# Optimization experiments

Measured on AMD Instinct MI355X. Metric: run time of the kernel, lower is better.

The kernel has to match this reference:

```python
import jax
import jax.numpy as jnp
from jax import lax
import numpy as np

DIM = 64
EPS = 1e-5
DN = ('NCDHW', 'OIDHW', 'NCDHW')


def setup_inputs() -> dict:
    key = jax.random.key(0)
    ks = jax.random.split(key, 4)
    x = jax.random.normal(ks[0], (2, DIM, 64, 64, 64), dtype=jnp.float32)
    gamma = jnp.ones((DIM,), jnp.float32)
    beta = jnp.zeros((DIM,), jnp.float32)
    w0 = jax.random.normal(ks[1], (DIM, 1, 5, 5, 5), jnp.float32) * 0.1
    b0 = jnp.zeros((DIM,), jnp.float32)
    ws = jax.random.normal(ks[2], (DIM, 1, 7, 7, 7), jnp.float32) * 0.05
    bs = jnp.zeros((DIM,), jnp.float32)
    w1 = jax.random.normal(ks[3], (DIM, DIM, 1, 1, 1), jnp.float32) * 0.1
    b1 = jnp.zeros((DIM,), jnp.float32)
    return {"x": x, "gamma": gamma, "beta": beta, "w0": w0, "b0": b0,
            "ws": ws, "bs": bs, "w1": w1, "b1": b1}


def _cb(b):
    # broadcast per-channel vector over NCDHW
    return b.reshape(1, -1, 1, 1, 1)


def reference(x, gamma, beta, w0, b0, ws, bs, w1, b1):
    dim = x.shape[1]
    # BatchNorm (training mode, biased variance) over N, D, H, W per channel
    mean = jnp.mean(x, axis=(0, 2, 3, 4), keepdims=True)
    var = jnp.var(x, axis=(0, 2, 3, 4), keepdims=True)
    xn = (x - mean) * lax.rsqrt(var + EPS) * _cb(gamma) + _cb(beta)
    # depthwise conv3d k=5, pad=2 (same)
    attn = lax.conv_general_dilated(xn, w0, (1, 1, 1), [(2, 2)] * 3,
                                    feature_group_count=dim,
                                    dimension_numbers=DN) + _cb(b0)
    # dilated depthwise conv3d k=7, dilation=3, pad=9 (same)
    attn = lax.conv_general_dilated(attn, ws, (1, 1, 1), [(9, 9)] * 3,
                                    rhs_dilation=(3, 3, 3),
                                    feature_group_count=dim,
                                    dimension_numbers=DN) + _cb(bs)
    # pointwise 1x1x1 conv
    attn = lax.conv_general_dilated(attn, w1, (1, 1, 1), [(0, 0)] * 3,
                                    dimension_numbers=DN) + _cb(b1)
    # gated multiply with residual input (u = x.clone())
    return x * attn
```

## Files before the change

### kernel.cpp

```cpp
#include <hip/hip_runtime.h>
#include <math.h>

#define C_DIM 64
#define N_B 2
#define SPATIAL (64*64*64)
#define PLANE_SZ (64*64)
#define EPSV 1e-5f

__global__ __launch_bounds__(256) void k_stats(const float* __restrict__ x,
                                               float* __restrict__ wsf) {
    int c = blockIdx.x >> 4;
    int part = blockIdx.x & 15;
    int tid = threadIdx.x;
    const int per_part = SPATIAL / 16;
    float s = 0.f, sq = 0.f;
    for (int n = 0; n < N_B; ++n) {
        const float* base = x + ((size_t)(n * C_DIM + c)) * SPATIAL + (size_t)part * per_part;
        const float4* b4 = (const float4*)base;
        #pragma unroll
        for (int it = 0; it < 16; ++it) {
            float4 v = b4[it * 256 + tid];
            s  += v.x + v.y + v.z + v.w;
            sq += v.x*v.x + v.y*v.y + v.z*v.z + v.w*v.w;
        }
    }
    __shared__ float rs[256], rq[256];
    rs[tid] = s; rq[tid] = sq;
    __syncthreads();
    for (int off = 128; off > 0; off >>= 1) {
        if (tid < off) { rs[tid] += rs[tid+off]; rq[tid] += rq[tid+off]; }
        __syncthreads();
    }
    if (tid == 0) {
        atomicAdd(&wsf[c], rs[0]);
        atomicAdd(&wsf[64 + c], rq[0]);
    }
}

__global__ void k_finalize(float* __restrict__ wsf,
                           const float* __restrict__ gamma,
                           const float* __restrict__ beta) {
    int c = threadIdx.x;
    float cnt = (float)(N_B * SPATIAL);
    float mean = wsf[c] / cnt;
    float var = wsf[64 + c] / cnt - mean * mean;
    float sc = gamma[c] * rsqrtf(var + EPSV);
    wsf[128 + c] = sc;
    wsf[192 + c] = beta[c] - mean * sc;
}

#define K2D 12
#define K2H 12
#define K2W 36
__global__ __launch_bounds__(256) void k_conv5(const float* __restrict__ x,
                                               const float* __restrict__ w0,
                                               const float* __restrict__ b0,
                                               const float* __restrict__ wsf,
                                               float* __restrict__ attn0) {
    __shared__ float sh[K2D * K2H * K2W];
    __shared__ float wt[125];
    int tid = threadIdx.x;
    int tx = tid & 31;
    int ty = tid >> 5;
    int wtile = blockIdx.x;
    int dt = blockIdx.y & 7;
    int ht = blockIdx.y >> 3;
    int nc = blockIdx.z;
    int c = nc & 63;
    int w0i = wtile * 32;
    int h0 = ht * 8;
    int d0 = dt * 8;
    const float* xb = x + (size_t)nc * SPATIAL;
    float sc = wsf[128 + c], shv = wsf[192 + c];
    if (tid < 125) wt[tid] = w0[c * 125 + tid];
    for (int idx = tid; idx < K2D * K2H * K2W; idx += 256) {
        int z = idx / (K2H * K2W);
        int rem = idx - z * (K2H * K2W);
        int y = rem / K2W;
        int xw = rem - y * K2W;
        int gd = d0 - 2 + z, gh = h0 - 2 + y, gw = w0i - 2 + xw;
        float v = 0.f;
        if ((unsigned)gd < 64u && (unsigned)gh < 64u && (unsigned)gw < 64u)
            v = xb[(size_t)gd * PLANE_SZ + gh * 64 + gw] * sc + shv;
        sh[idx] = v;
    }
    __syncthreads();
    float acc[8] = {0,0,0,0,0,0,0,0};
    #pragma unroll
    for (int z = 0; z < 12; ++z) {
        #pragma unroll
        for (int j = 0; j < 5; ++j) {
            #pragma unroll
            for (int k = 0; k < 5; ++k) {
                float v = sh[(z * K2H + (ty + j)) * K2W + tx + k];
                #pragma unroll
                for (int i = 0; i < 5; ++i) {
                    int dz = z - i;
                    if (dz >= 0 && dz < 8)
                        acc[dz] += wt[(i * 5 + j) * 5 + k] * v;
                }
            }
        }
    }
    float bias = b0[c];
    float* ob = attn0 + (size_t)nc * SPATIAL + (size_t)(h0 + ty) * 64 + w0i + tx;
    #pragma unroll
    for (int dz = 0; dz < 8; ++dz)
        ob[(size_t)(d0 + dz) * PLANE_SZ] = acc[dz] + bias;
}

#define ROWS7 22
#define COLS7 84

template<int P>
__device__ __forceinline__ void conv7_stage(const float* __restrict__ ab,
                                            const float* __restrict__ wc,
                                            float* __restrict__ sh,
                                            int tid, int hh, int w, int h0,
                                            int j0, int rd, float (&acc)[8]) {
    int m = j0 - 3 + P;
    int z = 3 * m + rd;
    bool zok = (m >= 0) && (z < 64);
    __syncthreads();
    if (zok) {
        const float* pb = ab + (size_t)z * PLANE_SZ;
        #pragma unroll
        for (int k = 0; k < 8; ++k) {
            int idx = k * 256 + tid;
            if (idx < ROWS7 * COLS7) {
                int row = idx / COLS7;
                int col = idx - row * COLS7;
                int gy = h0 - 9 + row;
                int gx = col - 9;
                float v = 0.f;
                if (col < 82 && (unsigned)gy < 64u && (unsigned)gx < 64u)
                    v = pb[gy * 64 + gx];
                sh[idx] = v;
            }
        }
    }
    __syncthreads();
    if (zok) {
        #pragma unroll
        for (int v = 0; v < 7; ++v) {
            float val[7];
            int rb = (hh + 3 * v) * COLS7 + w;
            #pragma unroll
            for (int u = 0; u < 7; ++u) val[u] = sh[rb + 3 * u];
            #pragma unroll
            for (int t = 0; t < 7; ++t) {
                const int q = P - t;
                if (q >= 0 && q < 8) {
                    #pragma unroll
                    for (int u = 0; u < 7; ++u)
                        acc[q] = fmaf(wc[t * 49 + v * 7 + u], val[u], acc[q]);
                }
            }
        }
    }
}

__global__ __launch_bounds__(256) void k_conv7(const float* __restrict__ attn0,
                                               const float* __restrict__ wsv,
                                               const float* __restrict__ bs,
                                               float* __restrict__ attn1) {
    __shared__ float sh[ROWS7 * COLS7];
    int tid = threadIdx.x;
    int w = tid & 63;
    int hh = tid >> 6;
    int ht = blockIdx.x;
    int rd = blockIdx.y % 3;
    int j0 = (blockIdx.y / 3) * 8;
    int nc = blockIdx.z;
    int c = nc & 63;
    int h0 = ht * 4;
    int h = h0 + hh;
    const float* ab = attn0 + (size_t)nc * SPATIAL;
    const float* wc = wsv + c * 343;
    float acc[8] = {0,0,0,0,0,0,0,0};

    conv7_stage< 0>(ab, wc, sh, tid, hh, w, h0, j0, rd, acc);
    conv7_stage< 1>(ab, wc, sh, tid, hh, w, h0, j0, rd, acc);
    conv7_stage< 2>(ab, wc, sh, tid, hh, w, h0, j0, rd, acc);
    conv7_stage< 3>(ab, wc, sh, tid, hh, w, h0, j0, rd, acc);
    conv7_stage< 4>(ab, wc, sh, tid, hh, w, h0, j0, rd, acc);
    conv7_stage< 5>(ab, wc, sh, tid, hh, w, h0, j0, rd, acc);
    conv7_stage< 6>(ab, wc, sh, tid, hh, w, h0, j0, rd, acc);
    conv7_stage< 7>(ab, wc, sh, tid, hh, w, h0, j0, rd, acc);
    conv7_stage< 8>(ab, wc, sh, tid, hh, w, h0, j0, rd, acc);
    conv7_stage< 9>(ab, wc, sh, tid, hh, w, h0, j0, rd, acc);
    conv7_stage<10>(ab, wc, sh, tid, hh, w, h0, j0, rd, acc);
    conv7_stage<11>(ab, wc, sh, tid, hh, w, h0, j0, rd, acc);
    conv7_stage<12>(ab, wc, sh, tid, hh, w, h0, j0, rd, acc);
    conv7_stage<13>(ab, wc, sh, tid, hh, w, h0, j0, rd, acc);

    float bias = bs[c];
    float* ob = attn1 + (size_t)nc * SPATIAL + (size_t)h * 64 + w;
    #pragma unroll
    for (int q = 0; q < 8; ++q) {
        int d = 3 * (j0 + q) + rd;
        if (d < 64)
            ob[(size_t)d * PLANE_SZ] = acc[q] + bias;
    }
}

__global__ __launch_bounds__(256) void k_pointwise(const float* __restrict__ attn1,
                                                   const float* __restrict__ x,
                                                   const float* __restrict__ w1,
                                                   const float* __restrict__ b1,
                                                   float* __restrict__ out) {
    __shared__ float at[64 * 64];
    int tid = threadIdx.x;
    int sl = tid & 63;
    int cg = __builtin_amdgcn_readfirstlane(tid >> 6);
    int s0 = blockIdx.x * 64;
    int n = blockIdx.y;
    const float* a_base = attn1 + (size_t)n * C_DIM * SPATIAL + s0;
    #pragma unroll
    for (int it = 0; it < 16; ++it) {
        int idx = it * 256 + tid;
        int row = idx >> 6;
        at[idx] = a_base[(size_t)row * SPATIAL + sl];
    }
    __syncthreads();
    float acc[16];
    #pragma unroll
    for (int j = 0; j < 16; ++j) acc[j] = 0.f;
    for (int ci = 0; ci < 64; ++ci) {
        float va = at[ci * 64 + sl];
        #pragma unroll
        for (int j = 0; j < 16; ++j) {
            int cc = cg * 16 + j;
            acc[j] += w1[cc * 64 + ci] * va;
        }
    }
    const float* xb = x + (size_t)n * C_DIM * SPATIAL + s0;
    float* ob = out + (size_t)n * C_DIM * SPATIAL + s0;
    #pragma unroll
    for (int j = 0; j < 16; ++j) {
        int cc = cg * 16 + j;
        float attn = acc[j] + b1[cc];
        ob[(size_t)cc * SPATIAL + sl] = xb[(size_t)cc * SPATIAL + sl] * attn;
    }
}

extern "C" void kernel_launch(void* const* d_in, const int* in_sizes, int n_in,
                              void* d_out, int out_size, void* d_ws, size_t ws_size,
                              hipStream_t stream) {
    const float* x     = (const float*)d_in[0];
    const float* gamma = (const float*)d_in[1];
    const float* beta  = (const float*)d_in[2];
    const float* w0    = (const float*)d_in[3];
    const float* b0    = (const float*)d_in[4];
    const float* wsv   = (const float*)d_in[5];
    const float* bs    = (const float*)d_in[6];
    const float* w1    = (const float*)d_in[7];
    const float* b1    = (const float*)d_in[8];
    float* out = (float*)d_out;
    float* wsf = (float*)d_ws;
    float* attn1 = wsf + 256;

    hipMemsetAsync(d_ws, 0, 1024, stream);
    k_stats<<<dim3(1024), dim3(256), 0, stream>>>(x, wsf);
    k_finalize<<<dim3(1), dim3(64), 0, stream>>>(wsf, gamma, beta);
    k_conv5<<<dim3(2, 64, 128), dim3(256), 0, stream>>>(x, w0, b0, wsf, out);
    k_conv7<<<dim3(16, 9, 128), dim3(256), 0, stream>>>(out, wsv, bs, attn1);
    k_pointwise<<<dim3(4096, 2), dim3(256), 0, stream>>>(attn1, x, w1, b1, out);
}
```

Before: 1.316 ms.

## Restructure dilated conv7 as depth-streaming sliding window with double-buffered planes

Rewrites the dilated 7x7x7 depthwise conv so each block owns one (rd, rh) dilation phase of a whole channel. It streams depth planes through double-buffered shared memory and keeps a 7-deep sliding accumulator per output, so every input plane is loaded once instead of once per output tile. Each thread now computes 4 strided rows, which reuses the values it loads across several outputs. The cost is far fewer blocks (9x128) with a large register footprint from 28 accumulators, which may hurt occupancy.

```diff
diff --git a/kernel.cpp b/kernel.cpp
--- a/kernel.cpp
+++ b/kernel.cpp
@@ -109,98 +109,121 @@
         ob[(size_t)(d0 + dz) * PLANE_SZ] = acc[dz] + bias;
 }
 
-#define ROWS7 22
+#define ROWS7 30
 #define COLS7 84
-
-template<int P>
-__device__ __forceinline__ void conv7_stage(const float* __restrict__ ab,
-                                            const float* __restrict__ wc,
-                                            float* __restrict__ sh,
-                                            int tid, int hh, int w, int h0,
-                                            int j0, int rd, float (&acc)[8]) {
-    int m = j0 - 3 + P;
-    int z = 3 * m + rd;
-    bool zok = (m >= 0) && (z < 64);
-    __syncthreads();
-    if (zok) {
-        const float* pb = ab + (size_t)z * PLANE_SZ;
-        #pragma unroll
-        for (int k = 0; k < 8; ++k) {
-            int idx = k * 256 + tid;
-            if (idx < ROWS7 * COLS7) {
-                int row = idx / COLS7;
-                int col = idx - row * COLS7;
-                int gy = h0 - 9 + row;
-                int gx = col - 9;
-                float v = 0.f;
-                if (col < 82 && (unsigned)gy < 64u && (unsigned)gx < 64u)
-                    v = pb[gy * 64 + gx];
-                sh[idx] = v;
-            }
-        }
-    }
-    __syncthreads();
-    if (zok) {
-        #pragma unroll
-        for (int v = 0; v < 7; ++v) {
+#define S7_T 384
+#define S7_ITERS 7
+#define S7_BUF (S7_ITERS * S7_T)
+
+__global__ __launch_bounds__(384, 4) void k_conv7(const float* __restrict__ attn0,
+                                                  const float* __restrict__ wsv,
+                                                  const float* __restrict__ bs,
+                                                  float* __restrict__ attn1) {
+    __shared__ float sh[2 * S7_BUF];
+    int tid = threadIdx.x;
+    int w  = tid & 63;
+    int th = tid >> 6;
+    int rh = blockIdx.x % 3;
+    int rd = blockIdx.x / 3;
+    int nc = blockIdx.y;
+    int c  = nc & 63;
+    const float* ab = attn0 + (size_t)nc * SPATIAL;
+    const float* wc = wsv + c * 343;
+    int M = (66 - rd) / 3;
+    int ah0 = th * 4;
+    int ahmax = (63 - rh) / 3;
+
+    int goff[S7_ITERS];
+    float gmsk[S7_ITERS];
+    #pragma unroll
+    for (int kk = 0; kk < S7_ITERS; ++kk) {
+        int idx = kk * S7_T + tid;
+        int row = idx / COLS7;
+        int e   = idx - row * COLS7;
+        int gy  = 3 * (row - 3) + rh;
+        int gx  = e - 9;
+        bool valid = (row < ROWS7) && ((unsigned)gy < 64u) && ((unsigned)gx < 64u);
+        goff[kk] = valid ? (gy * 64 + gx) : 0;
+        gmsk[kk] = valid ? 1.f : 0.f;
+    }
+
+    float acc[4][7];
+    #pragma unroll
+    for (int k = 0; k < 4; ++k)
+        #pragma unroll
+        for (int s = 0; s < 7; ++s) acc[k][s] = 0.f;
+
+    {
+        const float* pb = ab + (size_t)rd * PLANE_SZ;
+        #pragma unroll
+        for (int kk = 0; kk < S7_ITERS; ++kk)
+            sh[kk * S7_T + tid] = pb[goff[kk]] * gmsk[kk];
+    }
+    __syncthreads();
+
+    float bias = bs[c];
+    float* ob = attn1 + (size_t)nc * SPATIAL + (size_t)rd * PLANE_SZ
+              + (size_t)(3 * ah0 + rh) * 64 + w;
+    int rbase = ah0 * COLS7 + w;
+
+    for (int m = 0; m < M; ++m) {
+        const float* cur = sh + (m & 1) * S7_BUF;
+        float* nxt = sh + ((m + 1) & 1) * S7_BUF;
+        bool more = (m + 1 < M);
+        float r[S7_ITERS];
+        if (more) {
+            const float* pb = ab + (size_t)(3 * (m + 1) + rd) * PLANE_SZ;
+            #pragma unroll
+            for (int kk = 0; kk < S7_ITERS; ++kk)
+                r[kk] = pb[goff[kk]];
+        }
+        #pragma unroll
+        for (int jp = 0; jp < 10; ++jp) {
             float val[7];
-            int rb = (hh + 3 * v) * COLS7 + w;
-            #pragma unroll
-            for (int u = 0; u < 7; ++u) val[u] = sh[rb + 3 * u];
-            #pragma unroll
-            for (int t = 0; t < 7; ++t) {
-                const int q = P - t;
-                if (q >= 0 && q < 8) {
+            #pragma unroll
+            for (int u = 0; u < 7; ++u)
+                val[u] = cur[rbase + jp * COLS7 + 3 * u];
+            #pragma unroll
+            for (int k = 0; k < 4; ++k) {
+                const int v = jp - k;
+                if (v >= 0 && v < 7) {
                     #pragma unroll
-                    for (int u = 0; u < 7; ++u)
-                        acc[q] = fmaf(wc[t * 49 + v * 7 + u], val[u], acc[q]);
+                    for (int s = 0; s < 7; ++s) {
+                        #pragma unroll
+                        for (int u = 0; u < 7; ++u)
+                            acc[k][s] = fmaf(wc[(6 - s) * 49 + v * 7 + u],
+                                             val[u], acc[k][s]);
+                    }
                 }
             }
         }
-    }
-}
-
-__global__ __launch_bounds__(256) void k_conv7(const float* __restrict__ attn0,
-                                               const float* __restrict__ wsv,
-                                               const float* __restrict__ bs,
-                                               float* __restrict__ attn1) {
-    __shared__ float sh[ROWS7 * COLS7];
-    int tid = threadIdx.x;
-    int w = tid & 63;
-    int hh = tid >> 6;
-    int ht = blockIdx.x;
-    int rd = blockIdx.y % 3;
-    int j0 = (blockIdx.y / 3) * 8;
-    int nc = blockIdx.z;
-    int c = nc & 63;
-    int h0 = ht * 4;
-    int h = h0 + hh;
-    const float* ab = attn0 + (size_t)nc * SPATIAL;
-    const float* wc = wsv + c * 343;
-    float acc[8] = {0,0,0,0,0,0,0,0};
-
-    conv7_stage< 0>(ab, wc, sh, tid, hh, w, h0, j0, rd, acc);
-    conv7_stage< 1>(ab, wc, sh, tid, hh, w, h0, j0, rd, acc);
-    conv7_stage< 2>(ab, wc, sh, tid, hh, w, h0, j0, rd, acc);
-    conv7_stage< 3>(ab, wc, sh, tid, hh, w, h0, j0, rd, acc);
-    conv7_stage< 4>(ab, wc, sh, tid, hh, w, h0, j0, rd, acc);
-    conv7_stage< 5>(ab, wc, sh, tid, hh, w, h0, j0, rd, acc);
-    conv7_stage< 6>(ab, wc, sh, tid, hh, w, h0, j0, rd, acc);
-    conv7_stage< 7>(ab, wc, sh, tid, hh, w, h0, j0, rd, acc);
-    conv7_stage< 8>(ab, wc, sh, tid, hh, w, h0, j0, rd, acc);
-    conv7_stage< 9>(ab, wc, sh, tid, hh, w, h0, j0, rd, acc);
-    conv7_stage<10>(ab, wc, sh, tid, hh, w, h0, j0, rd, acc);
-    conv7_stage<11>(ab, wc, sh, tid, hh, w, h0, j0, rd, acc);
-    conv7_stage<12>(ab, wc, sh, tid, hh, w, h0, j0, rd, acc);
-    conv7_stage<13>(ab, wc, sh, tid, hh, w, h0, j0, rd, acc);
-
-    float bias = bs[c];
-    float* ob = attn1 + (size_t)nc * SPATIAL + (size_t)h * 64 + w;
-    #pragma unroll
-    for (int q = 0; q < 8; ++q) {
-        int d = 3 * (j0 + q) + rd;
-        if (d < 64)
-            ob[(size_t)d * PLANE_SZ] = acc[q] + bias;
+        if (m >= 3) {
+            #pragma unroll
+            for (int k = 0; k < 4; ++k)
+                if (ah0 + k <= ahmax)
+                    ob[k * 192] = acc[k][0] + bias;
+            ob += 3 * PLANE_SZ;
+        }
+        if (more) {
+            #pragma unroll
+            for (int kk = 0; kk < S7_ITERS; ++kk)
+                nxt[kk * S7_T + tid] = r[kk] * gmsk[kk];
+        }
+        __syncthreads();
+        #pragma unroll
+        for (int k = 0; k < 4; ++k) {
+            #pragma unroll
+            for (int s = 0; s < 6; ++s) acc[k][s] = acc[k][s + 1];
+            acc[k][6] = 0.f;
+        }
+    }
+    #pragma unroll
+    for (int s2 = 0; s2 < 3; ++s2) {
+        #pragma unroll
+        for (int k = 0; k < 4; ++k)
+            if (ah0 + k <= ahmax)
+                ob[k * 192] = acc[k][s2] + bias;
+        ob += 3 * PLANE_SZ;
     }
 }
 
@@ -264,6 +287,6 @@
     k_stats<<<dim3(1024), dim3(256), 0, stream>>>(x, wsf);
     k_finalize<<<dim3(1), dim3(64), 0, stream>>>(wsf, gamma, beta);
     k_conv5<<<dim3(2, 64, 128), dim3(256), 0, stream>>>(x, w0, b0, wsf, out);
-    k_conv7<<<dim3(16, 9, 128), dim3(256), 0, stream>>>(out, wsv, bs, attn1);
+    k_conv7<<<dim3(9, 128), dim3(384), 0, stream>>>(out, wsv, bs, attn1);
     k_pointwise<<<dim3(4096, 2), dim3(256), 0, stream>>>(attn1, x, w1, b1, out);
 }
```

New measurement: 2.115 ms. 60.7% more time.
